# Kernel optimization log

Measured on AMD Instinct MI355X. Metric: run time of the kernel, lower is better.

Reference implementation:

```python
import jax, jax.numpy as jnp
import numpy as np

NP, NM = 50, 32          # pathways, misc tokens
T = NP + NM              # 82 total tokens
D = 24                   # token_dim for latent_dim=2048: (2048//82)//4*4
H, DH, FF = 4, 6, 96     # heads, head_dim, ffn dim (4*D)
B = 8192
EPS = 1e-5


def _ln(x, g, b):
    m = x.mean(-1, keepdims=True)
    v = ((x - m) ** 2).mean(-1, keepdims=True)
    return (x - m) / jnp.sqrt(v + EPS) * g + b


def _adapter(x, w1, b1, g1, bb1, w2, b2, g2, bb2, w3, b3):
    # Linear -> LN -> GELU -> (Dropout eval) -> Linear -> LN -> GELU -> Linear
    h = jax.nn.gelu(_ln(x @ w1.T + b1, g1, bb1), approximate=False)
    h = jax.nn.gelu(_ln(h @ w2.T + b2, g2, bb2), approximate=False)
    return h @ w3.T + b3


def _enc_layer(x, wqkv, bqkv, wo, bo, lg1, lb1, fw1, fb1, fw2, fb2, lg2, lb2):
    # post-norm TransformerEncoderLayer (PyTorch defaults: relu FFN, batch_first)
    Bx, Tx, Dx = x.shape
    qkv = x @ wqkv.T + bqkv                       # [B,T,3D]
    q, k, v = jnp.split(qkv, 3, axis=-1)
    sh = lambda a: a.reshape(Bx, Tx, H, DH).transpose(0, 2, 1, 3)
    q, k, v = sh(q), sh(k), sh(v)
    att = jax.nn.softmax(jnp.einsum('bhqd,bhkd->bhqk', q, k) / jnp.sqrt(jnp.float32(DH)), axis=-1)
    o = jnp.einsum('bhqk,bhkd->bhqd', att, v).transpose(0, 2, 1, 3).reshape(Bx, Tx, Dx)
    o = o @ wo.T + bo
    x = _ln(x + o, lg1, lb1)
    f = jax.nn.relu(x @ fw1.T + fb1) @ fw2.T + fb2
    return _ln(x + f, lg2, lb2)


def setup_inputs() -> dict:
    key = jax.random.key(0)
    ks = iter(jax.random.split(key, 40))
    r = lambda *s: jax.random.normal(next(ks), s, dtype=jnp.float32) * 0.02
    inp = {
        'gene': jax.random.normal(next(ks), (B, 5000), dtype=jnp.float32),
        'protein': jax.random.normal(next(ks), (B, 226), dtype=jnp.float32),
        'pathway_tokens': jax.random.normal(next(ks), (NP, D), dtype=jnp.float32),
        'misc_tokens': jax.random.normal(next(ks), (NM, D), dtype=jnp.float32),
        # gene adapter: 5000 -> 512 -> 256 -> 82
        'gw1': r(512, 5000), 'gb1': jnp.zeros(512), 'gg1': jnp.ones(512), 'gbb1': jnp.zeros(512),
        'gw2': r(256, 512), 'gb2': jnp.zeros(256), 'gg2': jnp.ones(256), 'gbb2': jnp.zeros(256),
        'gw3': r(T, 256), 'gb3': jnp.zeros(T),
        # protein adapter: 226 -> 512 -> 256 -> 82
        'pw1': r(512, 226), 'pb1': jnp.zeros(512), 'pg1': jnp.ones(512), 'pbb1': jnp.zeros(512),
        'pw2': r(256, 512), 'pb2': jnp.zeros(256), 'pg2': jnp.ones(256), 'pbb2': jnp.zeros(256),
        'pw3': r(T, 256), 'pb3': jnp.zeros(T),
        # token mixer: 2 stacked TransformerEncoder layers
        'wqkv': r(2, 3 * D, D), 'bqkv': jnp.zeros((2, 3 * D)),
        'wo': r(2, D, D), 'bo': jnp.zeros((2, D)),
        'lg1': jnp.ones((2, D)), 'lb1': jnp.zeros((2, D)),
        'fw1': r(2, FF, D), 'fb1': jnp.zeros((2, FF)),
        'fw2': r(2, D, FF), 'fb2': jnp.zeros((2, D)),
        'lg2': jnp.ones((2, D)), 'lb2': jnp.zeros((2, D)),
    }
    return inp


def reference(gene, protein, pathway_tokens, misc_tokens,
              gw1, gb1, gg1, gbb1, gw2, gb2, gg2, gbb2, gw3, gb3,
              pw1, pb1, pg1, pbb1, pw2, pb2, pg2, pbb2, pw3, pb3,
              wqkv, bqkv, wo, bo, lg1, lb1, fw1, fb1, fw2, fb2, lg2, lb2):
    all_tokens = jnp.concatenate([pathway_tokens, misc_tokens], axis=0)    # [T,D]
    gene_w = jax.nn.softmax(_adapter(gene, gw1, gb1, gg1, gbb1, gw2, gb2, gg2, gbb2, gw3, gb3), axis=-1)
    prot_w = jax.nn.softmax(_adapter(protein, pw1, pb1, pg1, pbb1, pw2, pb2, pg2, pbb2, pw3, pb3), axis=-1)
    # vectorized form of the per-batch loop: token_activations[b] += all_tokens * w[b,:,None]
    acts = (gene_w + prot_w)[:, :, None] * all_tokens[None]               # [B,T,D]
    for l in range(2):
        acts = _enc_layer(acts, wqkv[l], bqkv[l], wo[l], bo[l], lg1[l], lb1[l],
                          fw1[l], fb1[l], fw2[l], fb2[l], lg2[l], lb2[l])
    return acts
```

## Files before the change

kernel.cpp:

```cpp
#include <hip/hip_runtime.h>
#include <hip/hip_bf16.h>
#include <math.h>

typedef __attribute__((ext_vector_type(4))) float f32x4;
typedef __attribute__((ext_vector_type(8))) short s16x8;
typedef __attribute__((ext_vector_type(4))) short s16x4;
typedef __attribute__((ext_vector_type(4))) unsigned int u32x4;
typedef __attribute__((ext_vector_type(2))) unsigned int u32x2;
typedef _Float16 h2 __attribute__((ext_vector_type(2)));

static __device__ __forceinline__ unsigned short f2bf(float f) {
  unsigned int u = __builtin_bit_cast(unsigned int, f);
  u += 0x7FFFu + ((u >> 16) & 1u);
  return (unsigned short)(u >> 16);
}
static __device__ __forceinline__ unsigned int pk2bf(float a, float b) {
  return (unsigned int)f2bf(a) | ((unsigned int)f2bf(b) << 16);
}
static __device__ __forceinline__ float bf2f(unsigned short u) {
  return __builtin_bit_cast(float, (unsigned int)u << 16);
}
static __device__ __forceinline__ float gelu_exact(float x) {
  return 0.5f * x * (1.0f + erff(x * 0.7071067811865475f));
}
static __device__ __forceinline__ h2 pkh2(float a, float b) {
#if __has_builtin(__builtin_amdgcn_cvt_pkrtz)
  return __builtin_bit_cast(h2, __builtin_amdgcn_cvt_pkrtz(a, b));
#else
  h2 r; r[0] = (_Float16)a; r[1] = (_Float16)b; return r;
#endif
}
static __device__ __forceinline__ float dot2u(h2 a, unsigned int b, float c) {
  h2 bh = __builtin_bit_cast(h2, b);
#if __has_builtin(__builtin_amdgcn_fdot2)
  return __builtin_amdgcn_fdot2(a, bh, c, false);
#else
  return fmaf((float)a[0], (float)bh[0], fmaf((float)a[1], (float)bh[1], c));
#endif
}
static __device__ __forceinline__ float exp2fast(float x) {
#if __has_builtin(__builtin_amdgcn_exp2f)
  return __builtin_amdgcn_exp2f(x);
#else
  return exp2f(x);
#endif
}
static __device__ __forceinline__ void gll16(const void* g, void* l) {
#if __has_builtin(__builtin_amdgcn_global_load_lds)
  __builtin_amdgcn_global_load_lds((__attribute__((address_space(1))) void*)(void*)g,
                                   (__attribute__((address_space(3))) void*)l, 16, 0, 0);
#else
  *(u32x4*)l = *(const u32x4*)g;
#endif
}

__global__ __launch_bounds__(256)
void convert_tile_kernel(const float* __restrict__ src, unsigned short* __restrict__ dst,
                         int Msrc, int Ksrc, int TK, int total16) {
  const int id = blockIdx.x * 256 + threadIdx.x;
  if (id >= total16) return;
  const int j = id & 511;
  const int tile = id >> 9;
  const int tk = tile % TK;
  const int tmm = tile / TK;
  const int r = j >> 3, cb = j & 7;
  const int lcb = cb ^ (r & 7);
  const int row = tmm * 64 + r;
  const int col = tk * 64 + lcb * 8;
  float v[8];
  #pragma unroll
  for (int i = 0; i < 8; ++i) v[i] = 0.f;
  if (row < Msrc) {
    const size_t base = (size_t)row * Ksrc + col;
    if (col + 8 <= Ksrc && ((base & 3) == 0)) {
      f32x4 a = *(const f32x4*)(src + base);
      f32x4 b = *(const f32x4*)(src + base + 4);
      v[0]=a[0];v[1]=a[1];v[2]=a[2];v[3]=a[3];
      v[4]=b[0];v[5]=b[1];v[6]=b[2];v[7]=b[3];
    } else {
      #pragma unroll
      for (int i = 0; i < 8; ++i) if (col + i < Ksrc) v[i] = src[base + i];
    }
  }
  u32x4 o = { pk2bf(v[0],v[1]), pk2bf(v[2],v[3]), pk2bf(v[4],v[5]), pk2bf(v[6],v[7]) };
  *(u32x4*)(dst + (size_t)id * 8) = o;
}

__global__ __launch_bounds__(256, 4)
void gemm_bf16t_kernel(const unsigned short* __restrict__ At, const unsigned short* __restrict__ Bt,
                       const float* __restrict__ bias, float* __restrict__ C,
                       int NT, int KT, int Ntrue, int Nld) {
  __shared__ unsigned short As[4096];
  __shared__ unsigned short Bs[8192];
  const int tid = threadIdx.x;
  const int lane = tid & 63;
  const int wid = tid >> 6;
  const int wm = wid >> 1, wn = wid & 1;
  const int lr = lane & 15;
  const int lkb = ((lane >> 4) & 3) * 16;
  const int l = blockIdx.x;
  const int xcd = l & 7;
  const int kl = l >> 3;
  const int nb = kl % NT;
// ... 86 lines not shown
    const size_t d16 = ((size_t)(tmv * TK + tk) << 9) + (r << 3) + (lcb ^ (r & 7));
    u32x4 o = { pk2bf(z[0],z[1]), pk2bf(z[2],z[3]), pk2bf(z[4],z[5]), pk2bf(z[6],z[7]) };
    *(u32x4*)(Y + d16 * 8) = o;
  } else {
    const int c0 = lane * 4;
    f32x4 a = *(const f32x4*)(xr + c0);
    float s = a[0]+a[1]+a[2]+a[3];
    float ss = a[0]*a[0]+a[1]*a[1]+a[2]*a[2]+a[3]*a[3];
    #pragma unroll
    for (int off = 1; off < 64; off <<= 1) { s += __shfl_xor(s, off); ss += __shfl_xor(ss, off); }
    const float mean = s * (1.f/256.f);
    const float var = ss * (1.f/256.f) - mean * mean;
    const float rstd = rsqrtf(var + 1e-5f);
    float z[4];
    #pragma unroll
    for (int i = 0; i < 4; ++i) z[i] = gelu_exact((a[i]-mean)*rstd*g[c0+i] + bta[c0+i]);
    const int tk = lane >> 4, lcb = (lane >> 1) & 7, half = lane & 1;
    const size_t d16 = ((size_t)(tmv * TK + tk) << 9) + (r << 3) + (lcb ^ (r & 7));
    u32x2 o = { pk2bf(z[0],z[1]), pk2bf(z[2],z[3]) };
    *(u32x2*)(Y + d16 * 8 + half * 4) = o;
  }
}

__global__ __launch_bounds__(256)
void softmax2_kernel(const float* __restrict__ la, const float* __restrict__ lp,
                     float* __restrict__ w, int B) {
  const int wid = threadIdx.x >> 6;
  const int lane = threadIdx.x & 63;
  const int row = blockIdx.x * 4 + wid;
  if (row >= B) return;
  const bool has2 = (lane < 18);
  const float* a = la + (size_t)row * 82;
  const float* p = lp + (size_t)row * 82;
  float a0 = a[lane], a1 = has2 ? a[64 + lane] : -1e30f;
  float m = fmaxf(a0, a1);
  #pragma unroll
  for (int off = 1; off < 64; off <<= 1) m = fmaxf(m, __shfl_xor(m, off));
  float ea0 = __expf(a0 - m);
  float ea1 = has2 ? __expf(a1 - m) : 0.f;
  float sa = ea0 + ea1;
  #pragma unroll
  for (int off = 1; off < 64; off <<= 1) sa += __shfl_xor(sa, off);
  float p0 = p[lane], p1 = has2 ? p[64 + lane] : -1e30f;
  float mp = fmaxf(p0, p1);
  #pragma unroll
  for (int off = 1; off < 64; off <<= 1) mp = fmaxf(mp, __shfl_xor(mp, off));
  float ep0 = __expf(p0 - mp);
  float ep1 = has2 ? __expf(p1 - mp) : 0.f;
  float sp = ep0 + ep1;
  #pragma unroll
  for (int off = 1; off < 64; off <<= 1) sp += __shfl_xor(sp, off);
  const float ia = 1.0f / sa, ip = 1.0f / sp;
  w[(size_t)row * 82 + lane] = ea0 * ia + ep0 * ip;
  if (has2) w[(size_t)row * 82 + 64 + lane] = ea1 * ia + ep1 * ip;
}

__global__ __launch_bounds__(256)
void pack_enc_kernel(const float* __restrict__ wqkv, const float* __restrict__ wo,
                     const float* __restrict__ fw1, const float* __restrict__ fw2,
                     unsigned short* __restrict__ dst) {
  const int i = blockIdx.x * 256 + threadIdx.x;
  if (i >= 19456) return;
  float v = 0.f;
  if (i < 5120) {
    const int l = i / 2560, r = (i % 2560) >> 5, k = i & 31;
    if (r < 72 && k < 24) v = wqkv[l * 1728 + r * 24 + k];
  } else if (i < 7168) {
    const int b2 = i - 5120; const int l = b2 / 1024, r = (b2 % 1024) >> 5, k = b2 & 31;
    if (r < 24 && k < 24) v = wo[l * 576 + r * 24 + k];
  } else if (i < 13312) {
    const int b2 = i - 7168; const int l = b2 / 3072, r = (b2 % 3072) >> 5, k = b2 & 31;
    if (k < 24) v = fw1[l * 2304 + r * 24 + k];
  } else {
    const int b2 = i - 13312; const int l = b2 / 3072, r = (b2 % 3072) / 96, h = b2 % 96;
    if (r < 24) v = fw2[l * 2304 + r * 96 + h];
  }
  dst[i] = f2bf(v);
}

#define TSTR 32
#define VSTR 96
#define LDS_SHORTS 36864

static __device__ __forceinline__ s16x8 frag32(const unsigned short* buf, int rowBase, int lane) {
  return *(const s16x8*)(buf + (rowBase + (lane & 15)) * TSTR + 8 * (lane >> 4));
}
static __device__ __forceinline__ s16x8 frag96(const unsigned short* buf, int rowBase, int kOff, int lane) {
  return *(const s16x8*)(buf + (rowBase + (lane & 15)) * VSTR + kOff + 8 * (lane >> 4));
}

__global__ __launch_bounds__(256, 2)
void encoder_mfma_kernel(const float* __restrict__ w_sum,
                         const float* __restrict__ pathway, const float* __restrict__ misc,
                         const unsigned short* __restrict__ wenc,
                         const float* __restrict__ bqkv, const float* __restrict__ bo,
                         const float* __restrict__ lg1, const float* __restrict__ lb1,
                         const float* __restrict__ fb1, const float* __restrict__ fb2,
                         const float* __restrict__ lg2, const float* __restrict__ lb2,
                         float* __restrict__ out, int Btot) {
  extern __shared__ unsigned short lds[];
  const int tid = threadIdx.x;
  const int lane = tid & 63;
  const int wv = tid >> 6;
  const int g = lane >> 4;
  const int c = lane & 15;
  const int q4 = g * 4;

  unsigned short* SA = lds + wv * 3072;
  unsigned short* SP = lds + 12288 + wv * 3072;
  unsigned short* SV = lds + 24576 + wv * 3072;
  const int b = blockIdx.x * 4 + wv;
  const int bb = (b < Btot) ? b : (Btot - 1);

  for (int s = lane; s < 384; s += 64) ((u32x4*)SP)[s] = (u32x4){0,0,0,0};
  for (int s = lane; s < 384; s += 64) ((u32x4*)SV)[s] = (u32x4){0,0,0,0};
  for (int r = lane; r < 96; r += 64) {
    unsigned short* dst = SA + r * TSTR;
    if (r < 82) {
      const float* trow = (r < 50) ? (pathway + r * 24) : (misc + (r - 50) * 24);
      const float wvv = w_sum[(size_t)bb * 82 + r];
      unsigned int d[12];
      #pragma unroll
      for (int k = 0; k < 6; ++k) {
        f32x4 v = *(const f32x4*)(trow + 4 * k);
        d[2*k]   = pk2bf(wvv * v[0], wvv * v[1]);
        d[2*k+1] = pk2bf(wvv * v[2], wvv * v[3]);
      }
      *(u32x4*)(dst)      = (u32x4){d[0],d[1],d[2],d[3]};
      *(u32x4*)(dst + 8)  = (u32x4){d[4],d[5],d[6],d[7]};
      *(u32x4*)(dst + 16) = (u32x4){d[8],d[9],d[10],d[11]};
    } else {
      *(u32x4*)(dst)      = (u32x4){0,0,0,0};
      *(u32x4*)(dst + 8)  = (u32x4){0,0,0,0};
      *(u32x4*)(dst + 16) = (u32x4){0,0,0,0};
    }
    *(u32x4*)(dst + 24) = (u32x4){0,0,0,0};
  }

  float xres[6][2][4];
  #pragma unroll
  for (int m = 0; m < 6; ++m)
    #pragma unroll
    for (int n = 0; n < 2; ++n)
      #pragma unroll
      for (int i = 0; i < 4; ++i)
        xres[m][n][i] = bf2f(SA[(16*m + q4 + i) * TSTR + 16*n + c]);
  s16x8 af[6];
  #pragma unroll
  for (int m = 0; m < 6; ++m) af[m] = frag32(SA, 16*m, lane);

  const float QS = 0.5889777913f;
  const f32x4 Z4 = (f32x4){0.f, 0.f, 0.f, 0.f};

  #pragma unroll 1
  for (int l = 0; l < 2; ++l) {
    const unsigned short* WQP = wenc + l * 2560;
    const unsigned short* WOP = wenc + 5120 + l * 1024;
    const unsigned short* F1P = wenc + 7168 + l * 3072;
    const unsigned short* F2P = wenc + 13312 + l * 3072;
    const float* bqv = bqkv + l * 72;

    #pragma unroll
    for (int tn = 0; tn < 5; ++tn) {
      s16x8 bq = frag32(WQP, 16 * tn, lane);
      f32x4 a6[6];
      #pragma unroll
      for (int tm = 0; tm < 6; ++tm)
        a6[tm] = __builtin_amdgcn_mfma_f32_16x16x32_bf16(af[tm], bq, Z4, 0, 0, 0);
      const int j = tn * 16 + c;
      const float bj = (j < 72) ? bqv[j] : 0.f;
      #pragma unroll
      for (int tm = 0; tm < 6; ++tm) {
        const int tokb = 16 * tm + q4;
        if (j < 24) {
          #pragma unroll
          for (int i = 0; i < 4; ++i)
            SP[(tokb + i) * TSTR + j] = f2bf((a6[tm][i] + bj) * QS);
        } else if (j < 48) {
          #pragma unroll
          for (int i = 0; i < 4; ++i)
            SA[(tokb + i) * TSTR + (j - 24)] = f2bf(a6[tm][i] + bj);
        } else if (j < 72) {
          u32x2 w = { pk2bf(a6[tm][0] + bj, a6[tm][1] + bj),
                      pk2bf(a6[tm][2] + bj, a6[tm][3] + bj) };
          *(u32x2*)(SV + (j - 48) * VSTR + tokb) = w;
        }
      }
    }
    s16x8 qf[6];
    #pragma unroll
    for (int n = 0; n < 6; ++n) qf[n] = frag32(SP, 16*n, lane);

    f32x4 ot[2][6];
    #pragma unroll
    for (int m = 0; m < 2; ++m)
      #pragma unroll
      for (int n = 0; n < 6; ++n) ot[m][n] = Z4;
    float lsum[6] = {0.f, 0.f, 0.f, 0.f, 0.f, 0.f};
    #pragma unroll
    for (int p = 0; p < 3; ++p) {
      s16x8 ka0 = frag32(SA, 32*p, lane);
      s16x8 ka1 = frag32(SA, 32*p + 16, lane);
      f32x4 st[2][6];
      #pragma unroll
      for (int n = 0; n < 6; ++n) {
        st[0][n] = __builtin_amdgcn_mfma_f32_16x16x32_bf16(ka0, qf[n], Z4, 0, 0, 0);
        st[1][n] = __builtin_amdgcn_mfma_f32_16x16x32_bf16(ka1, qf[n], Z4, 0, 0, 0);
      }
      #pragma unroll
      for (int m = 0; m < 2; ++m)
        #pragma unroll
        for (int n = 0; n < 6; ++n) {
          const int kbase = 32*p + 16*m + q4;
          float pv[4];
          #pragma unroll
          for (int i = 0; i < 4; ++i) {
            const float e = exp2fast(st[m][n][i]);
            pv[i] = (kbase + i < 82) ? e : 0.f;
            lsum[n] += pv[i];
          }
          u32x2 w = { pk2bf(pv[0], pv[1]), pk2bf(pv[2], pv[3]) };
          *(u32x2*)(SP + (16*n + c) * TSTR + 16*m + q4) = w;
        }
      s16x8 va0 = frag96(SV, 0, 32*p, lane);
      s16x8 va1 = frag96(SV, 16, 32*p, lane);
      #pragma unroll
      for (int n = 0; n < 6; ++n) {
        s16x8 pf = frag32(SP, 16*n, lane);
        ot[0][n] = __builtin_amdgcn_mfma_f32_16x16x32_bf16(va0, pf, ot[0][n], 0, 0, 0);
        ot[1][n] = __builtin_amdgcn_mfma_f32_16x16x32_bf16(va1, pf, ot[1][n], 0, 0, 0);
      }
    }
    #pragma unroll
    for (int n = 0; n < 6; ++n) {
      float lt = lsum[n];
      lt += __shfl_xor(lt, 16);
      lt += __shfl_xor(lt, 32);
      const float inv = 1.0f / lt;
      #pragma unroll
      for (int m = 0; m < 2; ++m) {
        f32x4 o = ot[m][n];
        u32x2 w = { pk2bf(o[0]*inv, o[1]*inv), pk2bf(o[2]*inv, o[3]*inv) };
        *(u32x2*)(SP + (16*n + c) * TSTR + 16*m + q4) = w;
      }
    }
    s16x8 wof0 = frag32(WOP, 0, lane);
    s16x8 wof1 = frag32(WOP, 16, lane);
    const float bo0 = bo[l*24 + c];
    const float bo1 = (c < 8) ? bo[l*24 + 16 + c] : 0.f;
    const float g10 = lg1[l*24 + c];
    const float g11 = (c < 8) ? lg1[l*24 + 16 + c] : 0.f;
    const float be0 = lb1[l*24 + c];
    const float be1 = (c < 8) ? lb1[l*24 + 16 + c] : 0.f;
    float xn[6][2][4];
    #pragma unroll
    for (int m = 0; m < 6; ++m) {
      s16x8 oa = frag32(SP, 16*m, lane);
      f32x4 x0 = __builtin_amdgcn_mfma_f32_16x16x32_bf16(oa, wof0, Z4, 0, 0, 0);
      f32x4 x1 = __builtin_amdgcn_mfma_f32_16x16x32_bf16(oa, wof1, Z4, 0, 0, 0);
      #pragma unroll
      for (int i = 0; i < 4; ++i) {
        const float v0 = x0[i] + bo0 + xres[m][0][i];
        const float v1 = ((c < 8) ? (x1[i] + bo1) : 0.f) + xres[m][1][i];
        float s = v0 + v1;
        s += __shfl_xor(s, 1); s += __shfl_xor(s, 2);
        s += __shfl_xor(s, 4); s += __shfl_xor(s, 8);
        const float mu = s * (1.f / 24.f);
        const float d0 = v0 - mu;
        const float d1 = (c < 8) ? (v1 - mu) : 0.f;
        float vr = d0 * d0 + d1 * d1;
        vr += __shfl_xor(vr, 1); vr += __shfl_xor(vr, 2);
        vr += __shfl_xor(vr, 4); vr += __shfl_xor(vr, 8);
        const float rstd = rsqrtf(vr * (1.f / 24.f) + 1e-5f);
        xn[m][0][i] = d0 * rstd * g10 + be0;
        xn[m][1][i] = (c < 8) ? (d1 * rstd * g11 + be1) : 0.f;
      }
    }
    #pragma unroll
    for (int m = 0; m < 6; ++m)
      #pragma unroll
      for (int n = 0; n < 2; ++n)
        #pragma unroll
        for (int i = 0; i < 4; ++i)
          SP[(16*m + q4 + i) * TSTR + 16*n + c] = f2bf(xn[m][n][i]);
    s16x8 xnb[6];
    #pragma unroll
    for (int n = 0; n < 6; ++n) xnb[n] = frag32(SP, 16*n, lane);
    f32x4 ya[6][2];
    #pragma unroll
    for (int m = 0; m < 6; ++m) { ya[m][0] = Z4; ya[m][1] = Z4; }
    const float* fb1v = fb1 + l * 96;
    #pragma unroll
    for (int hp = 0; hp < 3; ++hp) {
      s16x8 f1a0 = frag32(F1P, 32*hp, lane);
      s16x8 f1a1 = frag32(F1P, 32*hp + 16, lane);
      #pragma unroll
      for (int n = 0; n < 6; ++n) {
        f32x4 h0 = __builtin_amdgcn_mfma_f32_16x16x32_bf16(f1a0, xnb[n], Z4, 0, 0, 0);
        f32x4 h1 = __builtin_amdgcn_mfma_f32_16x16x32_bf16(f1a1, xnb[n], Z4, 0, 0, 0);
        const int hb0 = 32*hp + q4, hb1 = 32*hp + 16 + q4;
        float r0[4], r1[4];
        #pragma unroll
        for (int i = 0; i < 4; ++i) {
          r0[i] = fmaxf(h0[i] + fb1v[hb0 + i], 0.f);
          r1[i] = fmaxf(h1[i] + fb1v[hb1 + i], 0.f);
        }
        u32x2 w0 = { pk2bf(r0[0], r0[1]), pk2bf(r0[2], r0[3]) };
        u32x2 w1 = { pk2bf(r1[0], r1[1]), pk2bf(r1[2], r1[3]) };
        *(u32x2*)(SA + (16*n + c) * TSTR + q4) = w0;
        *(u32x2*)(SA + (16*n + c) * TSTR + 16 + q4) = w1;
      }
      s16x8 f2f0 = frag96(F2P, 0, 32*hp, lane);
      s16x8 f2f1 = frag96(F2P, 16, 32*hp, lane);
      #pragma unroll
      for (int m = 0; m < 6; ++m) {
        s16x8 ha = frag32(SA, 16*m, lane);
        ya[m][0] = __builtin_amdgcn_mfma_f32_16x16x32_bf16(ha, f2f0, ya[m][0], 0, 0, 0);
        ya[m][1] = __builtin_amdgcn_mfma_f32_16x16x32_bf16(ha, f2f1, ya[m][1], 0, 0, 0);
      }
    }
    const float fb20 = fb2[l*24 + c];
    const float fb21 = (c < 8) ? fb2[l*24 + 16 + c] : 0.f;
    const float g20 = lg2[l*24 + c];
    const float g21 = (c < 8) ? lg2[l*24 + 16 + c] : 0.f;
    const float be20 = lb2[l*24 + c];
    const float be21 = (c < 8) ? lb2[l*24 + 16 + c] : 0.f;
    float xf[6][2][4];
    #pragma unroll
    for (int m = 0; m < 6; ++m)
      #pragma unroll
      for (int i = 0; i < 4; ++i) {
        const float v0 = ya[m][0][i] + fb20 + xn[m][0][i];
        const float v1 = ((c < 8) ? (ya[m][1][i] + fb21) : 0.f) + xn[m][1][i];
        float s = v0 + v1;
        s += __shfl_xor(s, 1); s += __shfl_xor(s, 2);
        s += __shfl_xor(s, 4); s += __shfl_xor(s, 8);
        const float mu = s * (1.f / 24.f);
        const float d0 = v0 - mu;
        const float d1 = (c < 8) ? (v1 - mu) : 0.f;
        float vr = d0 * d0 + d1 * d1;
        vr += __shfl_xor(vr, 1); vr += __shfl_xor(vr, 2);
        vr += __shfl_xor(vr, 4); vr += __shfl_xor(vr, 8);
        const float rstd = rsqrtf(vr * (1.f / 24.f) + 1e-5f);
        xf[m][0][i] = d0 * rstd * g20 + be20;
        xf[m][1][i] = (c < 8) ? (d1 * rstd * g21 + be21) : 0.f;
      }
    if (l == 0) {
      #pragma unroll
      for (int m = 0; m < 6; ++m)
        #pragma unroll
        for (int n = 0; n < 2; ++n)
          #pragma unroll
          for (int i = 0; i < 4; ++i) {
            SA[(16*m + q4 + i) * TSTR + 16*n + c] = f2bf(xf[m][n][i]);
            xres[m][n][i] = xf[m][n][i];
          }
      #pragma unroll
      for (int m = 0; m < 6; ++m) af[m] = frag32(SA, 16*m, lane);
    } else if (b < Btot) {
      #pragma unroll
      for (int m = 0; m < 6; ++m)
        #pragma unroll
        for (int i = 0; i < 4; ++i) {
          const int q = 16*m + q4 + i;
          if (q < 82) {
            out[(size_t)b * 1968 + q * 24 + c] = xf[m][0][i];
            if (c < 8) out[(size_t)b * 1968 + q * 24 + 16 + c] = xf[m][1][i];
          }
        }
    }
  }
}

#define GBM 64
#define GBN 128
#define GBK 64
#define GLDS 72

__global__ __launch_bounds__(256, 2)
void gemm_bias_kernel(const float* __restrict__ A, const float* __restrict__ Bw,
                      const float* __restrict__ bias, float* __restrict__ C,
                      int M, int N, int K) {
  __shared__ short As[GBM * GLDS];
  __shared__ short Bs[GBN * GLDS];
  const int tid = threadIdx.x;
  const int lane = tid & 63;
  const int wid = tid >> 6;
  const int wm = wid >> 1;
  const int wn = wid & 1;
  const int m0 = blockIdx.x * GBM;
  const int n0 = blockIdx.y * GBN;
  const int lr = lane & 15;
  const int lk = (lane >> 4) * 8;
  const bool kAligned = ((K & 3) == 0);
  f32x4 acc[2][4];
  #pragma unroll
  for (int i = 0; i < 2; ++i)
    #pragma unroll
    for (int j = 0; j < 4; ++j) acc[i][j] = (f32x4){0.f, 0.f, 0.f, 0.f};
  for (int k0 = 0; k0 < K; k0 += GBK) {
    __syncthreads();
    const bool fullK = kAligned && (k0 + GBK <= K);
    #pragma unroll
    for (int pass = 0; pass < 4; ++pass) {
      const int f = pass * 1024 + tid * 4;
      const int r = f >> 6, cc = f & 63;
      f32x4 v = (f32x4){0.f, 0.f, 0.f, 0.f};
      const float* src = A + (size_t)(m0 + r) * K + (k0 + cc);
      if (fullK) v = *(const f32x4*)src;
      else {
        #pragma unroll
        for (int i = 0; i < 4; ++i) if (k0 + cc + i < K) v[i] = src[i];
      }
      s16x4 sv = { (short)f2bf(v[0]), (short)f2bf(v[1]), (short)f2bf(v[2]), (short)f2bf(v[3]) };
      *(s16x4*)&As[r * GLDS + cc] = sv;
    }
    #pragma unroll
    for (int pass = 0; pass < 8; ++pass) {
      const int f = pass * 1024 + tid * 4;
      const int r = f >> 6, cc = f & 63;
      f32x4 v = (f32x4){0.f, 0.f, 0.f, 0.f};
      if (n0 + r < N) {
        const float* src = Bw + (size_t)(n0 + r) * K + (k0 + cc);
        if (fullK) v = *(const f32x4*)src;
        else {
          #pragma unroll
          for (int i = 0; i < 4; ++i) if (k0 + cc + i < K) v[i] = src[i];
        }
      }
      s16x4 sv = { (short)f2bf(v[0]), (short)f2bf(v[1]), (short)f2bf(v[2]), (short)f2bf(v[3]) };
      *(s16x4*)&Bs[r * GLDS + cc] = sv;
    }
    __syncthreads();
    #pragma unroll
    for (int kk = 0; kk < GBK; kk += 32) {
      s16x8 af2[2], bfr[4];
      #pragma unroll
      for (int m = 0; m < 2; ++m)
        af2[m] = *(const s16x8*)&As[(wm * 32 + m * 16 + lr) * GLDS + kk + lk];
      #pragma unroll
      for (int n = 0; n < 4; ++n)
        bfr[n] = *(const s16x8*)&Bs[(wn * 64 + n * 16 + lr) * GLDS + kk + lk];
      #pragma unroll
      for (int m = 0; m < 2; ++m)
        #pragma unroll
        for (int n = 0; n < 4; ++n)
          acc[m][n] = __builtin_amdgcn_mfma_f32_16x16x32_bf16(af2[m], bfr[n], acc[m][n], 0, 0, 0);
    }
  }
  const int crow = (lane >> 4) * 4;
  #pragma unroll
  for (int m = 0; m < 2; ++m) {
// ... 236 lines not shown
      float sa = Bf1[2*jp], sb = Bf1[2*jp+1];
      const unsigned int* w1 = F1h + (2*jp) * 12;
      #pragma unroll
      for (int kd = 0; kd < 12; ++kd) { sa = dot2u(xnh[kd], w1[kd], sa); sb = dot2u(xnh[kd], w1[12 + kd], sb); }
      sa = fmaxf(sa, 0.f);
      sb = fmaxf(sb, 0.f);
      h2 sp = pkh2(sa, sb);
      const unsigned int* w2 = F2t + jp * 24;
      #pragma unroll
      for (int d = 0; d < 24; ++d) y[d] = dot2u(sp, w2[d], y[d]);
    }
    float mean2 = 0.f;
    #pragma unroll
    for (int j = 0; j < 24; ++j) mean2 += y[j];
    mean2 *= (1.f / 24.f);
    float var2 = 0.f;
    #pragma unroll
    for (int j = 0; j < 24; ++j) { const float dd = y[j] - mean2; var2 = fmaf(dd, dd, var2); }
    var2 *= (1.f / 24.f);
    const float rstd2 = rsqrtf(var2 + 1e-5f);
    const float* G2 = lg2 + layer * 24;
    const float* Bl2 = lb2 + layer * 24;
    #pragma unroll
    for (int j = 0; j < 24; ++j) xf[j] = (y[j] - mean2) * rstd2 * G2[j] + Bl2[j];
    if (layer == 0) {
      #pragma unroll
      for (int j = 0; j < 24; ++j) x[j] = xf[j];
    }
    __syncthreads();
  }
  if (storeOK) {
    float* op = out + (size_t)b * 1968 + t * 24;
    #pragma unroll
    for (int d4 = 0; d4 < 6; ++d4) {
      f32x4 v = { xf[4*d4], xf[4*d4+1], xf[4*d4+2], xf[4*d4+3] };
      *(f32x4*)(op + 4 * d4) = v;
    }
  }
}

extern "C" void kernel_launch(void* const* d_in, const int* in_sizes, int n_in,
                              void* d_out, int out_size, void* d_ws, size_t ws_size,
                              hipStream_t stream) {
  const float* gene    = (const float*)d_in[0];
  const float* protein = (const float*)d_in[1];
  const float* pathway = (const float*)d_in[2];
  const float* misc    = (const float*)d_in[3];
  const float* gw1 = (const float*)d_in[4];
  const float* gb1 = (const float*)d_in[5];
  const float* gg1 = (const float*)d_in[6];
  const float* gbb1= (const float*)d_in[7];
  const float* gw2 = (const float*)d_in[8];
  const float* gb2 = (const float*)d_in[9];
  const float* gg2 = (const float*)d_in[10];
  const float* gbb2= (const float*)d_in[11];
  const float* gw3 = (const float*)d_in[12];
  const float* gb3 = (const float*)d_in[13];
  const float* pw1 = (const float*)d_in[14];
  const float* pb1 = (const float*)d_in[15];
  const float* pg1 = (const float*)d_in[16];
  const float* pbb1= (const float*)d_in[17];
  const float* pw2 = (const float*)d_in[18];
  const float* pb2 = (const float*)d_in[19];
  const float* pg2 = (const float*)d_in[20];
  const float* pbb2= (const float*)d_in[21];
  const float* pw3 = (const float*)d_in[22];
  const float* pb3 = (const float*)d_in[23];
  const float* wqkv= (const float*)d_in[24];
  const float* bqkv= (const float*)d_in[25];
  const float* wo  = (const float*)d_in[26];
  const float* bo  = (const float*)d_in[27];
  const float* lg1 = (const float*)d_in[28];
  const float* lb1 = (const float*)d_in[29];
  const float* fw1 = (const float*)d_in[30];
  const float* fb1 = (const float*)d_in[31];
  const float* fw2 = (const float*)d_in[32];
  const float* fb2 = (const float*)d_in[33];
  const float* lg2 = (const float*)d_in[34];
  const float* lb2 = (const float*)d_in[35];

  const int B = in_sizes[0] / 5000;
  dim3 blk(256);

  static int mfma_lds_ok = -1;
  if (mfma_lds_ok < 0) {
    hipError_t e = hipFuncSetAttribute((const void*)encoder_mfma_kernel,
        hipFuncAttributeMaxDynamicSharedMemorySize, LDS_SHORTS * 2);
    mfma_lds_ok = 1;
    (void)e;
  }

  size_t off = 0;
  auto take = [&](size_t bytes) { size_t r = off; off = (off + bytes + 255) & ~(size_t)255; return r; };
  const size_t o_geneB  = take((size_t)B * 5056 * 2);
  const size_t o_protB  = take((size_t)B * 256 * 2);
  const size_t o_gw1B   = take((size_t)512 * 5056 * 2);
  const size_t o_pw1B   = take((size_t)512 * 256 * 2);
  const size_t o_gw2B   = take((size_t)256 * 512 * 2);
  const size_t o_pw2B   = take((size_t)256 * 512 * 2);
  const size_t o_gw3B   = take((size_t)128 * 256 * 2);
  const size_t o_pw3B   = take((size_t)128 * 256 * 2);
  const size_t o_Cbuf   = take((size_t)B * 512 * 4);
  const size_t o_h1B    = take((size_t)B * 512 * 2);
  const size_t o_h2B    = take((size_t)B * 256 * 2);
  const size_t o_lg     = take((size_t)B * 82 * 4);
  const size_t o_lp     = take((size_t)B * 82 * 4);
  const size_t o_wsum   = take((size_t)B * 82 * 4);
  const size_t o_wenc   = take((size_t)19456 * 2);
  const size_t need = off;

  if (need <= ws_size) {
    char* base = (char*)d_ws;
    unsigned short* geneB = (unsigned short*)(base + o_geneB);
    unsigned short* protB = (unsigned short*)(base + o_protB);
    unsigned short* gw1B  = (unsigned short*)(base + o_gw1B);
    unsigned short* pw1B  = (unsigned short*)(base + o_pw1B);
    unsigned short* gw2B  = (unsigned short*)(base + o_gw2B);
    unsigned short* pw2B  = (unsigned short*)(base + o_pw2B);
    unsigned short* gw3B  = (unsigned short*)(base + o_gw3B);
    unsigned short* pw3B  = (unsigned short*)(base + o_pw3B);
    float* Cbuf = (float*)(base + o_Cbuf);
    unsigned short* h1B = (unsigned short*)(base + o_h1B);
    unsigned short* h2B = (unsigned short*)(base + o_h2B);
    float* logits_g = (float*)(base + o_lg);
    float* logits_p = (float*)(base + o_lp);
    float* w_sum    = (float*)(base + o_wsum);
    unsigned short* wenc = (unsigned short*)(base + o_wenc);

    const int MT = B / 64;
    pack_enc_kernel<<<dim3(76), blk, 0, stream>>>(wqkv, wo, fw1, fw2, wenc);
    {
      int t16 = MT * 79 * 512;
      convert_tile_kernel<<<dim3((t16 + 255) / 256), blk, 0, stream>>>(gene, geneB, B, 5000, 79, t16);
      t16 = MT * 4 * 512;
      convert_tile_kernel<<<dim3((t16 + 255) / 256), blk, 0, stream>>>(protein, protB, B, 226, 4, t16);
      t16 = 8 * 79 * 512;
      convert_tile_kernel<<<dim3((t16 + 255) / 256), blk, 0, stream>>>(gw1, gw1B, 512, 5000, 79, t16);
      t16 = 8 * 4 * 512;
      convert_tile_kernel<<<dim3((t16 + 255) / 256), blk, 0, stream>>>(pw1, pw1B, 512, 226, 4, t16);
      t16 = 4 * 8 * 512;
      convert_tile_kernel<<<dim3((t16 + 255) / 256), blk, 0, stream>>>(gw2, gw2B, 256, 512, 8, t16);
      convert_tile_kernel<<<dim3((t16 + 255) / 256), blk, 0, stream>>>(pw2, pw2B, 256, 512, 8, t16);
      t16 = 2 * 4 * 512;
      convert_tile_kernel<<<dim3((t16 + 255) / 256), blk, 0, stream>>>(gw3, gw3B, 82, 256, 4, t16);
      convert_tile_kernel<<<dim3((t16 + 255) / 256), blk, 0, stream>>>(pw3, pw3B, 82, 256, 4, t16);
    }
    gemm_bf16t_kernel<<<dim3(MT * 4), blk, 0, stream>>>(geneB, gw1B, gb1, Cbuf, 4, 79, 512, 512);
    ln_gelu_b16t_kernel<<<dim3(B / 4), blk, 0, stream>>>(Cbuf, gg1, gbb1, h1B, 512, 8);
    gemm_bf16t_kernel<<<dim3(MT * 2), blk, 0, stream>>>(h1B, gw2B, gb2, Cbuf, 2, 8, 256, 256);
    ln_gelu_b16t_kernel<<<dim3(B / 4), blk, 0, stream>>>(Cbuf, gg2, gbb2, h2B, 256, 4);
    gemm_bf16t_kernel<<<dim3(MT * 1), blk, 0, stream>>>(h2B, gw3B, gb3, logits_g, 1, 4, 82, 82);
    gemm_bf16t_kernel<<<dim3(MT * 4), blk, 0, stream>>>(protB, pw1B, pb1, Cbuf, 4, 4, 512, 512);
    ln_gelu_b16t_kernel<<<dim3(B / 4), blk, 0, stream>>>(Cbuf, pg1, pbb1, h1B, 512, 8);
    gemm_bf16t_kernel<<<dim3(MT * 2), blk, 0, stream>>>(h1B, pw2B, pb2, Cbuf, 2, 8, 256, 256);
    ln_gelu_b16t_kernel<<<dim3(B / 4), blk, 0, stream>>>(Cbuf, pg2, pbb2, h2B, 256, 4);
    gemm_bf16t_kernel<<<dim3(MT * 1), blk, 0, stream>>>(h2B, pw3B, pb3, logits_p, 1, 4, 82, 82);
    softmax2_kernel<<<dim3((B + 3) / 4), blk, 0, stream>>>(logits_g, logits_p, w_sum, B);
    encoder_mfma_kernel<<<dim3((B + 3) / 4), blk, LDS_SHORTS * 2, stream>>>(
        w_sum, pathway, misc, wenc, bqkv, bo, lg1, lb1,
        fb1, fb2, lg2, lb2, (float*)d_out, B);
    return;
  }

  float* bufA = (float*)d_ws;
  float* bufB = bufA + (size_t)B * 512;
  float* logits_g = bufB + (size_t)B * 512;
  float* logits_p = logits_g + (size_t)B * 82;
  float* w_sum    = logits_p + (size_t)B * 82;
  unsigned int* whb = (unsigned int*)(w_sum + (size_t)B * 82);

  pack_weights_kernel<<<dim3(27), blk, 0, stream>>>(wqkv, wo, fw1, fw2, whb);
  gemm_bias_kernel<<<dim3(B / 64, 4), blk, 0, stream>>>(gene, gw1, gb1, bufA, B, 512, 5000);
  ln_gelu_kernel<<<dim3(B), blk, 0, stream>>>(bufA, gg1, gbb1, bufB, 512);
// ... 13 lines not shown
```

Baseline: 630.8 us.

## Swizzle encoder LDS tiles and pack residual registers as bf16 pairs

Applies an XOR swizzle to the per-wave LDS token tiles (SA, SP, SV) so the 16-row MFMA fragment reads and the transposed scatter writes spread across more banks. The fp32 residual and post-norm arrays are kept as packed bf16 pairs in registers instead of fp32, which cuts register pressure in the encoder kernel. The residual now goes through bf16 rounding, which changes numerics slightly. The one-time hipFuncSetAttribute guard is removed, so the call now runs on every launch.

```diff
diff --git a/kernel.cpp b/kernel.cpp
--- a/kernel.cpp
+++ b/kernel.cpp
@@ -19,6 +19,12 @@
 }
 static __device__ __forceinline__ float bf2f(unsigned short u) {
   return __builtin_bit_cast(float, (unsigned int)u << 16);
+}
+static __device__ __forceinline__ float bfloU(unsigned int u) {
+  return __builtin_bit_cast(float, u << 16);
+}
+static __device__ __forceinline__ float bfhiU(unsigned int u) {
+  return __builtin_bit_cast(float, u & 0xFFFF0000u);
 }
 static __device__ __forceinline__ float gelu_exact(float x) {
   return 0.5f * x * (1.0f + erff(x * 0.7071067811865475f));
@@ -271,11 +277,25 @@
 #define VSTR 96
 #define LDS_SHORTS 36864
 
-static __device__ __forceinline__ s16x8 frag32(const unsigned short* buf, int rowBase, int lane) {
-  return *(const s16x8*)(buf + (rowBase + (lane & 15)) * TSTR + 8 * (lane >> 4));
-}
-static __device__ __forceinline__ s16x8 frag96(const unsigned short* buf, int rowBase, int kOff, int lane) {
-  return *(const s16x8*)(buf + (rowBase + (lane & 15)) * VSTR + kOff + 8 * (lane >> 4));
+static __device__ __forceinline__ int sidx(int row, int col) {
+  return row * TSTR + (col ^ (((row >> 1) & 3) << 3));
+}
+static __device__ __forceinline__ int vidx(int row, int col) {
+  return row * VSTR + (col ^ (((row >> 1) & 3) << 3));
+}
+static __device__ __forceinline__ s16x8 frag32g(const unsigned short* buf, int rowBase, int lane) {
+  return *(const s16x8*)(buf + (rowBase + (lane & 15)) * 32 + 8 * (lane >> 4));
+}
+static __device__ __forceinline__ s16x8 frag96g(const unsigned short* buf, int rowBase, int kOff, int lane) {
+  return *(const s16x8*)(buf + (rowBase + (lane & 15)) * 96 + kOff + 8 * (lane >> 4));
+}
+static __device__ __forceinline__ s16x8 frag32s(const unsigned short* buf, int rowBase, int lane) {
+  const int r = rowBase + (lane & 15);
+  return *(const s16x8*)(buf + sidx(r, 8 * (lane >> 4)));
+}
+static __device__ __forceinline__ s16x8 frag96s(const unsigned short* buf, int rowBase, int kOff, int lane) {
+  const int r = rowBase + (lane & 15);
+  return *(const s16x8*)(buf + vidx(r, kOff + 8 * (lane >> 4)));
 }
 
 __global__ __launch_bounds__(256, 2)
@@ -304,7 +324,6 @@
   for (int s = lane; s < 384; s += 64) ((u32x4*)SP)[s] = (u32x4){0,0,0,0};
   for (int s = lane; s < 384; s += 64) ((u32x4*)SV)[s] = (u32x4){0,0,0,0};
   for (int r = lane; r < 96; r += 64) {
-    unsigned short* dst = SA + r * TSTR;
     if (r < 82) {
       const float* trow = (r < 50) ? (pathway + r * 24) : (misc + (r - 50) * 24);
       const float wvv = w_sum[(size_t)bb * 82 + r];
@@ -315,28 +334,29 @@
         d[2*k]   = pk2bf(wvv * v[0], wvv * v[1]);
         d[2*k+1] = pk2bf(wvv * v[2], wvv * v[3]);
       }
-      *(u32x4*)(dst)      = (u32x4){d[0],d[1],d[2],d[3]};
-      *(u32x4*)(dst + 8)  = (u32x4){d[4],d[5],d[6],d[7]};
-      *(u32x4*)(dst + 16) = (u32x4){d[8],d[9],d[10],d[11]};
+      *(u32x4*)(SA + sidx(r, 0))  = (u32x4){d[0],d[1],d[2],d[3]};
+      *(u32x4*)(SA + sidx(r, 8))  = (u32x4){d[4],d[5],d[6],d[7]};
+      *(u32x4*)(SA + sidx(r, 16)) = (u32x4){d[8],d[9],d[10],d[11]};
     } else {
-      *(u32x4*)(dst)      = (u32x4){0,0,0,0};
-      *(u32x4*)(dst + 8)  = (u32x4){0,0,0,0};
-      *(u32x4*)(dst + 16) = (u32x4){0,0,0,0};
-    }
-    *(u32x4*)(dst + 24) = (u32x4){0,0,0,0};
-  }
-
-  float xres[6][2][4];
+      *(u32x4*)(SA + sidx(r, 0))  = (u32x4){0,0,0,0};
+      *(u32x4*)(SA + sidx(r, 8))  = (u32x4){0,0,0,0};
+      *(u32x4*)(SA + sidx(r, 16)) = (u32x4){0,0,0,0};
+    }
+    *(u32x4*)(SA + sidx(r, 24)) = (u32x4){0,0,0,0};
+  }
+
+  unsigned int xresp[6][4];
   #pragma unroll
   for (int m = 0; m < 6; ++m)
     #pragma unroll
-    for (int n = 0; n < 2; ++n)
-      #pragma unroll
-      for (int i = 0; i < 4; ++i)
-        xres[m][n][i] = bf2f(SA[(16*m + q4 + i) * TSTR + 16*n + c]);
+    for (int i = 0; i < 4; ++i) {
+      const int row = 16*m + q4 + i;
+      xresp[m][i] = (unsigned int)SA[sidx(row, c)] |
+                    ((unsigned int)SA[sidx(row, 16 + c)] << 16);
+    }
   s16x8 af[6];
   #pragma unroll
-  for (int m = 0; m < 6; ++m) af[m] = frag32(SA, 16*m, lane);
+  for (int m = 0; m < 6; ++m) af[m] = frag32s(SA, 16*m, lane);
 
   const float QS = 0.5889777913f;
   const f32x4 Z4 = (f32x4){0.f, 0.f, 0.f, 0.f};
@@ -351,7 +371,7 @@
 
     #pragma unroll
     for (int tn = 0; tn < 5; ++tn) {
-      s16x8 bq = frag32(WQP, 16 * tn, lane);
+      s16x8 bq = frag32g(WQP, 16 * tn, lane);
       f32x4 a6[6];
       #pragma unroll
       for (int tm = 0; tm < 6; ++tm)
@@ -364,21 +384,21 @@
         if (j < 24) {
           #pragma unroll
           for (int i = 0; i < 4; ++i)
-            SP[(tokb + i) * TSTR + j] = f2bf((a6[tm][i] + bj) * QS);
+            SP[sidx(tokb + i, j)] = f2bf((a6[tm][i] + bj) * QS);
         } else if (j < 48) {
           #pragma unroll
           for (int i = 0; i < 4; ++i)
-            SA[(tokb + i) * TSTR + (j - 24)] = f2bf(a6[tm][i] + bj);
+            SA[sidx(tokb + i, j - 24)] = f2bf(a6[tm][i] + bj);
         } else if (j < 72) {
           u32x2 w = { pk2bf(a6[tm][0] + bj, a6[tm][1] + bj),
                       pk2bf(a6[tm][2] + bj, a6[tm][3] + bj) };
-          *(u32x2*)(SV + (j - 48) * VSTR + tokb) = w;
+          *(u32x2*)(SV + vidx(j - 48, tokb)) = w;
         }
       }
     }
     s16x8 qf[6];
     #pragma unroll
-    for (int n = 0; n < 6; ++n) qf[n] = frag32(SP, 16*n, lane);
+    for (int n = 0; n < 6; ++n) qf[n] = frag32s(SP, 16*n, lane);
 
     f32x4 ot[2][6];
     #pragma unroll
@@ -388,8 +408,8 @@
     float lsum[6] = {0.f, 0.f, 0.f, 0.f, 0.f, 0.f};
     #pragma unroll
     for (int p = 0; p < 3; ++p) {
-      s16x8 ka0 = frag32(SA, 32*p, lane);
-      s16x8 ka1 = frag32(SA, 32*p + 16, lane);
+      s16x8 ka0 = frag32s(SA, 32*p, lane);
+      s16x8 ka1 = frag32s(SA, 32*p + 16, lane);
       f32x4 st[2][6];
       #pragma unroll
       for (int n = 0; n < 6; ++n) {
@@ -409,13 +429,13 @@
             lsum[n] += pv[i];
           }
           u32x2 w = { pk2bf(pv[0], pv[1]), pk2bf(pv[2], pv[3]) };
-          *(u32x2*)(SP + (16*n + c) * TSTR + 16*m + q4) = w;
+          *(u32x2*)(SP + sidx(16*n + c, 16*m + q4)) = w;
         }
-      s16x8 va0 = frag96(SV, 0, 32*p, lane);
-      s16x8 va1 = frag96(SV, 16, 32*p, lane);
+      s16x8 va0 = frag96s(SV, 0, 32*p, lane);
+      s16x8 va1 = frag96s(SV, 16, 32*p, lane);
       #pragma unroll
       for (int n = 0; n < 6; ++n) {
-        s16x8 pf = frag32(SP, 16*n, lane);
+        s16x8 pf = frag32s(SP, 16*n, lane);
         ot[0][n] = __builtin_amdgcn_mfma_f32_16x16x32_bf16(va0, pf, ot[0][n], 0, 0, 0);
         ot[1][n] = __builtin_amdgcn_mfma_f32_16x16x32_bf16(va1, pf, ot[1][n], 0, 0, 0);
       }
@@ -430,27 +450,27 @@
       for (int m = 0; m < 2; ++m) {
         f32x4 o = ot[m][n];
         u32x2 w = { pk2bf(o[0]*inv, o[1]*inv), pk2bf(o[2]*inv, o[3]*inv) };
-        *(u32x2*)(SP + (16*n + c) * TSTR + 16*m + q4) = w;
-      }
-    }
-    s16x8 wof0 = frag32(WOP, 0, lane);
-    s16x8 wof1 = frag32(WOP, 16, lane);
+        *(u32x2*)(SP + sidx(16*n + c, 16*m + q4)) = w;
+      }
+    }
+    s16x8 wof0 = frag32g(WOP, 0, lane);
+    s16x8 wof1 = frag32g(WOP, 16, lane);
     const float bo0 = bo[l*24 + c];
     const float bo1 = (c < 8) ? bo[l*24 + 16 + c] : 0.f;
     const float g10 = lg1[l*24 + c];
     const float g11 = (c < 8) ? lg1[l*24 + 16 + c] : 0.f;
     const float be0 = lb1[l*24 + c];
     const float be1 = (c < 8) ? lb1[l*24 + 16 + c] : 0.f;
-    float xn[6][2][4];
+    unsigned int xnp[6][4];
     #pragma unroll
     for (int m = 0; m < 6; ++m) {
-      s16x8 oa = frag32(SP, 16*m, lane);
+      s16x8 oa = frag32s(SP, 16*m, lane);
       f32x4 x0 = __builtin_amdgcn_mfma_f32_16x16x32_bf16(oa, wof0, Z4, 0, 0, 0);
       f32x4 x1 = __builtin_amdgcn_mfma_f32_16x16x32_bf16(oa, wof1, Z4, 0, 0, 0);
       #pragma unroll
       for (int i = 0; i < 4; ++i) {
-        const float v0 = x0[i] + bo0 + xres[m][0][i];
-        const float v1 = ((c < 8) ? (x1[i] + bo1) : 0.f) + xres[m][1][i];
+        const float v0 = x0[i] + bo0 + bfloU(xresp[m][i]);
+        const float v1 = ((c < 8) ? (x1[i] + bo1) : 0.f) + bfhiU(xresp[m][i]);
         float s = v0 + v1;
         s += __shfl_xor(s, 1); s += __shfl_xor(s, 2);
         s += __shfl_xor(s, 4); s += __shfl_xor(s, 8);
@@ -461,28 +481,30 @@
         vr += __shfl_xor(vr, 1); vr += __shfl_xor(vr, 2);
         vr += __shfl_xor(vr, 4); vr += __shfl_xor(vr, 8);
         const float rstd = rsqrtf(vr * (1.f / 24.f) + 1e-5f);
-        xn[m][0][i] = d0 * rstd * g10 + be0;
-        xn[m][1][i] = (c < 8) ? (d1 * rstd * g11 + be1) : 0.f;
+        const float n0 = d0 * rstd * g10 + be0;
+        const float n1 = (c < 8) ? (d1 * rstd * g11 + be1) : 0.f;
+        xnp[m][i] = pk2bf(n0, n1);
       }
     }
     #pragma unroll
     for (int m = 0; m < 6; ++m)
       #pragma unroll
-      for (int n = 0; n < 2; ++n)
-        #pragma unroll
-        for (int i = 0; i < 4; ++i)
-          SP[(16*m + q4 + i) * TSTR + 16*n + c] = f2bf(xn[m][n][i]);
+      for (int i = 0; i < 4; ++i) {
+        const int row = 16*m + q4 + i;
+        SP[sidx(row, c)]      = (unsigned short)(xnp[m][i] & 0xFFFFu);
+        SP[sidx(row, 16 + c)] = (unsigned short)(xnp[m][i] >> 16);
+      }
     s16x8 xnb[6];
     #pragma unroll
-    for (int n = 0; n < 6; ++n) xnb[n] = frag32(SP, 16*n, lane);
+    for (int n = 0; n < 6; ++n) xnb[n] = frag32s(SP, 16*n, lane);
     f32x4 ya[6][2];
     #pragma unroll
     for (int m = 0; m < 6; ++m) { ya[m][0] = Z4; ya[m][1] = Z4; }
     const float* fb1v = fb1 + l * 96;
     #pragma unroll
     for (int hp = 0; hp < 3; ++hp) {
-      s16x8 f1a0 = frag32(F1P, 32*hp, lane);
-      s16x8 f1a1 = frag32(F1P, 32*hp + 16, lane);
+      s16x8 f1a0 = frag32g(F1P, 32*hp, lane);
+      s16x8 f1a1 = frag32g(F1P, 32*hp + 16, lane);
       #pragma unroll
       for (int n = 0; n < 6; ++n) {
         f32x4 h0 = __builtin_amdgcn_mfma_f32_16x16x32_bf16(f1a0, xnb[n], Z4, 0, 0, 0);
@@ -496,14 +518,14 @@
         }
         u32x2 w0 = { pk2bf(r0[0], r0[1]), pk2bf(r0[2], r0[3]) };
         u32x2 w1 = { pk2bf(r1[0], r1[1]), pk2bf(r1[2], r1[3]) };
-        *(u32x2*)(SA + (16*n + c) * TSTR + q4) = w0;
-        *(u32x2*)(SA + (16*n + c) * TSTR + 16 + q4) = w1;
-      }
-      s16x8 f2f0 = frag96(F2P, 0, 32*hp, lane);
-      s16x8 f2f1 = frag96(F2P, 16, 32*hp, lane);
+        *(u32x2*)(SA + sidx(16*n + c, q4)) = w0;
+        *(u32x2*)(SA + sidx(16*n + c, 16 + q4)) = w1;
+      }
+      s16x8 f2f0 = frag96g(F2P, 0, 32*hp, lane);
+      s16x8 f2f1 = frag96g(F2P, 16, 32*hp, lane);
       #pragma unroll
       for (int m = 0; m < 6; ++m) {
-        s16x8 ha = frag32(SA, 16*m, lane);
+        s16x8 ha = frag32s(SA, 16*m, lane);
         ya[m][0] = __builtin_amdgcn_mfma_f32_16x16x32_bf16(ha, f2f0, ya[m][0], 0, 0, 0);
         ya[m][1] = __builtin_amdgcn_mfma_f32_16x16x32_bf16(ha, f2f1, ya[m][1], 0, 0, 0);
       }
@@ -514,13 +536,12 @@
     const float g21 = (c < 8) ? lg2[l*24 + 16 + c] : 0.f;
     const float be20 = lb2[l*24 + c];
     const float be21 = (c < 8) ? lb2[l*24 + 16 + c] : 0.f;
-    float xf[6][2][4];
     #pragma unroll
     for (int m = 0; m < 6; ++m)
       #pragma unroll
       for (int i = 0; i < 4; ++i) {
-        const float v0 = ya[m][0][i] + fb20 + xn[m][0][i];
-        const float v1 = ((c < 8) ? (ya[m][1][i] + fb21) : 0.f) + xn[m][1][i];
+        const float v0 = ya[m][0][i] + fb20 + bfloU(xnp[m][i]);
+        const float v1 = ((c < 8) ? (ya[m][1][i] + fb21) : 0.f) + bfhiU(xnp[m][i]);
         float s = v0 + v1;
         s += __shfl_xor(s, 1); s += __shfl_xor(s, 2);
         s += __shfl_xor(s, 4); s += __shfl_xor(s, 8);
@@ -531,32 +552,24 @@
         vr += __shfl_xor(vr, 1); vr += __shfl_xor(vr, 2);
         vr += __shfl_xor(vr, 4); vr += __shfl_xor(vr, 8);
         const float rstd = rsqrtf(vr * (1.f / 24.f) + 1e-5f);
-        xf[m][0][i] = d0 * rstd * g20 + be20;
-        xf[m][1][i] = (c < 8) ? (d1 * rstd * g21 + be21) : 0.f;
-      }
-    if (l == 0) {
-      #pragma unroll
-      for (int m = 0; m < 6; ++m)
-        #pragma unroll
-        for (int n = 0; n < 2; ++n)
-          #pragma unroll
-          for (int i = 0; i < 4; ++i) {
-            SA[(16*m + q4 + i) * TSTR + 16*n + c] = f2bf(xf[m][n][i]);
-            xres[m][n][i] = xf[m][n][i];
-          }
-      #pragma unroll
-      for (int m = 0; m < 6; ++m) af[m] = frag32(SA, 16*m, lane);
-    } else if (b < Btot) {
-      #pragma unroll
-      for (int m = 0; m < 6; ++m)
-        #pragma unroll
-        for (int i = 0; i < 4; ++i) {
+        const float f0 = d0 * rstd * g20 + be20;
+        const float f1 = (c < 8) ? (d1 * rstd * g21 + be21) : 0.f;
+        if (l == 0) {
+          const int row = 16*m + q4 + i;
+          SA[sidx(row, c)]      = f2bf(f0);
+          SA[sidx(row, 16 + c)] = f2bf(f1);
+          xresp[m][i] = pk2bf(f0, f1);
+        } else if (b < Btot) {
           const int q = 16*m + q4 + i;
           if (q < 82) {
-            out[(size_t)b * 1968 + q * 24 + c] = xf[m][0][i];
-            if (c < 8) out[(size_t)b * 1968 + q * 24 + 16 + c] = xf[m][1][i];
+            out[(size_t)b * 1968 + q * 24 + c] = f0;
+            if (c < 8) out[(size_t)b * 1968 + q * 24 + 16 + c] = f1;
           }
         }
+      }
+    if (l == 0) {
+      #pragma unroll
+      for (int m = 0; m < 6; ++m) af[m] = frag32s(SA, 16*m, lane);
     }
   }
 }
@@ -959,13 +972,8 @@
   const int B = in_sizes[0] / 5000;
   dim3 blk(256);
 
-  static int mfma_lds_ok = -1;
-  if (mfma_lds_ok < 0) {
-    hipError_t e = hipFuncSetAttribute((const void*)encoder_mfma_kernel,
-        hipFuncAttributeMaxDynamicSharedMemorySize, LDS_SHORTS * 2);
-    mfma_lds_ok = 1;
-    (void)e;
-  }
+  (void)hipFuncSetAttribute((const void*)encoder_mfma_kernel,
+      hipFuncAttributeMaxDynamicSharedMemorySize, LDS_SHORTS * 2);
 
   size_t off = 0;
   auto take = [&](size_t bytes) { size_t r = off; off = (off + bytes + 255) & ~(size_t)255; return r; };
```

After: 678.7 us. 1.08x slower.
